# Optimization experiments

Measured on AMD Instinct MI355X. Metric: run time of the kernel, lower is better.

Reference implementation:

```python
import jax, jax.numpy as jnp
import numpy as np
import math

NH, NKV, HD = 8, 1, 128
SOFTCAP = 30.0
ROPE_BASE = 500000.0


def _rope_tables(T, hd, base):
    half = hd // 2
    inv_freq = 1.0 / (base ** (np.arange(half, dtype=np.float32) / half))
    t = np.arange(T, dtype=np.float32)
    ang = np.outer(t, inv_freq)  # [T, half]
    return jnp.asarray(np.cos(ang)), jnp.asarray(np.sin(ang))


def apply_rope(x, cos, sin):
    # x: [B, T, H, hd]; cos/sin: [T, hd//2]
    half = x.shape[-1] // 2
    x1, x2 = x[..., :half], x[..., half:]
    T = x.shape[1]
    c = cos[:T][None, :, None, :]
    s = sin[:T][None, :, None, :]
    return jnp.concatenate([x1 * c - x2 * s, x1 * s + x2 * c], axis=-1)


def setup_inputs() -> dict:
    key = jax.random.key(0)
    ks = jax.random.split(key, 5)
    B, T, D = 4, 2048, 1024
    KD = NKV * HD
    x = jax.random.normal(ks[0], (B, T, D), dtype=jnp.float32)
    Wq = jax.random.normal(ks[1], (D, D), dtype=jnp.float32) * (D ** -0.5)
    Wk = jax.random.normal(ks[2], (KD, D), dtype=jnp.float32) * (D ** -0.5)
    Wv = jax.random.normal(ks[3], (KD, D), dtype=jnp.float32) * (D ** -0.5)
    Wo = jax.random.normal(ks[4], (D, D), dtype=jnp.float32) * (D ** -0.5)
    qk_gain = jnp.full((NH,), 1.5, dtype=jnp.float32)  # qk_gain_init
    cos, sin = _rope_tables(T, HD, ROPE_BASE)
    return {"x": x, "Wq": Wq, "Wk": Wk, "Wv": Wv, "Wo": Wo,
            "qk_gain": qk_gain, "cos": cos, "sin": sin}


def reference(x, Wq, Wk, Wv, Wo, qk_gain, cos, sin):
    B, T, D = x.shape
    # projections (QuantLinear with qat disabled == plain linear, no bias)
    q = (x @ Wq.T).reshape(B, T, NH, HD)
    k = (x @ Wk.T).reshape(B, T, NKV, HD)
    v = (x @ Wv.T).reshape(B, T, NKV, HD)
    q = apply_rope(q, cos, sin)
    k = apply_rope(k, cos, sin)
    # learned per-head QK gain applied to queries
    q = q * qk_gain[None, None, :, 1 - 1][..., None] if False else q * qk_gain[None, None, :, None]
    # GQA: broadcast the single kv head across NH query heads
    scale = 1.0 / math.sqrt(HD)
    scores = jnp.einsum('bqhd,bkgd->bhqk', q, k) * scale  # g==NKV==1 broadcast
    # logit softcap before masking/softmax
    scores = SOFTCAP * jnp.tanh(scores / SOFTCAP)
    causal = jnp.tril(jnp.ones((T, T), dtype=bool))
    scores = jnp.where(causal[None, None], scores, -jnp.inf)
    attn = jax.nn.softmax(scores, axis=-1)  # [B, NH, T, T]
    out = jnp.einsum('bhqk,bkgd->bqhd', attn, v).reshape(B, T, NH * HD)
    return out @ Wo.T
```

## Files before the change

kernel.cpp:

```cpp
#include <hip/hip_runtime.h>
#include <hip/hip_bf16.h>

#define B_ 4
#define T_ 2048
#define D_ 1024
#define NH_ 8
#define HD_ 128

typedef short short8 __attribute__((ext_vector_type(8)));
typedef float floatx4 __attribute__((ext_vector_type(4)));

#if __has_builtin(__builtin_amdgcn_exp2f)
#define EXP2F __builtin_amdgcn_exp2f
#else
#define EXP2F exp2f
#endif
#if __has_builtin(__builtin_amdgcn_rcpf)
#define RCPF __builtin_amdgcn_rcpf
#else
__device__ __forceinline__ float RCPF(float x) { return 1.f / x; }
#endif

#if __has_builtin(__builtin_amdgcn_global_load_lds)
#define G2L(gp, lp)                                                        \
  __builtin_amdgcn_global_load_lds(                                        \
      (const __attribute__((address_space(1))) unsigned int*)(gp),         \
      (__attribute__((address_space(3))) unsigned int*)(lp), 16, 0, 0)
#else
#define G2L(gp, lp) (*(uint4*)(lp) = *(const uint4*)(gp))
#endif

__device__ __forceinline__ unsigned short f2b(float f) {
  union { float fl; unsigned int i; } v; v.fl = f;
  unsigned int r = v.i + 0x7fffu + ((v.i >> 16) & 1u);
  return (unsigned short)(r >> 16);
}
__device__ __forceinline__ unsigned int pack_bf16(float a, float b) {
  unsigned int ua = __float_as_uint(a) + 0x8000u;
  unsigned int ub = __float_as_uint(b) + 0x8000u;
  return (ua >> 16) | (ub & 0xffff0000u);
}
__device__ __forceinline__ float blo(unsigned int u) { return __uint_as_float(u << 16); }
__device__ __forceinline__ float bhi(unsigned int u) { return __uint_as_float(u & 0xffff0000u); }

__global__ __launch_bounds__(256) void cvt_kernel(
    const float* __restrict__ x,  const float* __restrict__ wq,
    const float* __restrict__ wk, const float* __restrict__ wv,
    const float* __restrict__ wo, unsigned short* __restrict__ dst)
{
  size_t i = ((size_t)blockIdx.x * 256 + threadIdx.x) * 8;
  const float* src; size_t off;
  if      (i <  8388608u) { src = x;  off = i; }
  else if (i <  9437184u) { src = wq; off = i - 8388608u; }
  else if (i <  9568256u) { src = wk; off = i - 9437184u; }
  else if (i <  9699328u) { src = wv; off = i - 9568256u; }
  else                    { src = wo; off = i - 9699328u; }
  float4 a = *(const float4*)(src + off);
  float4 b = *(const float4*)(src + off + 4);
  uint4 o;
  o.x = pack_bf16(a.x, a.y); o.y = pack_bf16(a.z, a.w);
  o.z = pack_bf16(b.x, b.y); o.w = pack_bf16(b.z, b.w);
  *(uint4*)(dst + i) = o;
}

template <bool C_F32>
__device__ __forceinline__ void gemm_body_1024(
    const unsigned short* __restrict__ Arow0,
    const unsigned short* __restrict__ Btile,
    void* __restrict__ Cb, int ldC)
{
  __shared__ unsigned short As[128 * 32];
  __shared__ unsigned short Bs[128 * 32];
  const int tid = threadIdx.x;
  const int lane = tid & 63;
  const int w = tid >> 6;
  const int wr = w >> 1, wc = w & 1;
  const int l15 = lane & 15, quad = lane >> 4;

  const unsigned short* a_src = Arow0 + (size_t)(tid >> 2) * 1024 + (tid & 3) * 8;
  const unsigned short* b_src = Btile + (size_t)(tid >> 2) * 1024 + (tid & 3) * 8;
  unsigned short* a_dst = &As[(tid >> 2) * 32 + (tid & 3) * 8];
  unsigned short* b_dst = &Bs[(tid >> 2) * 32 + (tid & 3) * 8];

  floatx4 zero = {0.f, 0.f, 0.f, 0.f};
  floatx4 acc[4][4];
#pragma unroll
  for (int i = 0; i < 4; i++)
#pragma unroll
    for (int j = 0; j < 4; j++) acc[i][j] = zero;

  for (int k0 = 0; k0 < 1024; k0 += 32) {
    __syncthreads();
    G2L(a_src + k0,         a_dst);
    G2L(a_src + 65536 + k0, a_dst + 2048);
    G2L(b_src + k0,         b_dst);
    G2L(b_src + 65536 + k0, b_dst + 2048);
    __syncthreads();
    short8 af[4], bfr[4];
#pragma unroll
    for (int i = 0; i < 4; i++)
      af[i] = *(const short8*)&As[(wr * 64 + i * 16 + l15) * 32 + quad * 8];
#pragma unroll
    for (int j = 0; j < 4; j++)
      bfr[j] = *(const short8*)&Bs[(wc * 64 + j * 16 + l15) * 32 + quad * 8];
#pragma unroll
    for (int i = 0; i < 4; i++)
#pragma unroll
      for (int j = 0; j < 4; j++)
        acc[i][j] = __builtin_amdgcn_mfma_f32_16x16x32_bf16(af[i], bfr[j], acc[i][j], 0, 0, 0);
  }
#pragma unroll
  for (int i = 0; i < 4; i++)
#pragma unroll
    for (int j = 0; j < 4; j++)
#pragma unroll
      for (int r = 0; r < 4; r++) {
        size_t off = (size_t)(wr * 64 + i * 16 + quad * 4 + r) * ldC + wc * 64 + j * 16 + l15;
        if (C_F32) ((float*)Cb)[off] = acc[i][j][r];
        else ((unsigned short*)Cb)[off] = f2b(acc[i][j][r]);
      }
}

__global__ __launch_bounds__(256) void gemm_qkv_kernel(
    const unsigned short* __restrict__ x,
    const unsigned short* __restrict__ Wq,
    const unsigned short* __restrict__ Wk,
    const unsigned short* __restrict__ Wv,
    unsigned short* __restrict__ q,
    unsigned short* __restrict__ k,
    unsigned short* __restrict__ v)
{
  const int bx = blockIdx.x, by = blockIdx.y;
  const unsigned short* Btile;
  unsigned short* C;
  int ldC, col0;
  if (by < 8) { Btile = Wq + (size_t)by * 128 * 1024; C = q; ldC = 1024; col0 = by * 128; }
  else if (by == 8) { Btile = Wk; C = k; ldC = 128; col0 = 0; }
  else { Btile = Wv; C = v; ldC = 128; col0 = 0; }
  gemm_body_1024<false>(x + (size_t)bx * 128 * 1024, Btile,
                        C + (size_t)bx * 128 * ldC + col0, ldC);
}

__global__ __launch_bounds__(256) void gemm_out_kernel(
    const unsigned short* __restrict__ ao,
    const unsigned short* __restrict__ Wo,
    float* __restrict__ out)
{
  const int bx = blockIdx.x, by = blockIdx.y;
  gemm_body_1024<true>(ao + (size_t)bx * 128 * 1024, Wo + (size_t)by * 128 * 1024,
                       out + (size_t)bx * 128 * 1024 + by * 128, 1024);
}

__global__ __launch_bounds__(256) void prep_kernel(
    unsigned short* __restrict__ q,
    unsigned short* __restrict__ k,
    const unsigned short* __restrict__ v,
    unsigned short* __restrict__ vT,
    const float* __restrict__ cosT,
    const float* __restrict__ sinT,
    const float* __restrict__ gain)
{
  __shared__ unsigned short tile[32 * 136];
  const int tid = threadIdx.x;
  if (blockIdx.x < 256) {
    const int b = blockIdx.x >> 6, t0 = (blockIdx.x & 63) * 32;
    for (int u = tid; u < 512; u += 256) {
      int r = u >> 4, c = u & 15;
      *(uint4*)&tile[r * 136 + c * 8] =
          *(const uint4*)(v + ((size_t)(b * T_ + t0 + r)) * 128 + c * 8);
    }
    __syncthreads();
    for (int u = tid; u < 512; u += 256) {
      int d = u >> 2, c = u & 3;
      short8 val;
#pragma unroll
      for (int j = 0; j < 8; j++) val[j] = (short)tile[(c * 8 + j) * 136 + d];
      *(short8*)(vT + ((size_t)(b * 128 + d)) * T_ + t0 + c * 8) = val;
    }
    return;
  }
  int idx = (blockIdx.x - 256) * 256 + tid;
  unsigned short* ptr;
  size_t base;
  int t, j;
  float g;
  if (idx < 524288) {
    j = idx & 7;
    int h = (idx >> 3) & 7;
    int bt = idx >> 6;
    t = bt & (T_ - 1);
    base = (size_t)bt * 1024 + h * 128 + j * 8;
    ptr = q;
    g = gain[h] * 0.0029462782549439484f;
  } else {
    int id = idx - 524288;
    j = id & 7;
    int bt = id >> 3;
    t = bt & (T_ - 1);
    base = (size_t)bt * 128 + j * 8;
    ptr = k;
    g = 1.f;
  }
  float4 ca = *(const float4*)&cosT[t * 64 + j * 8];
  float4 cb = *(const float4*)&cosT[t * 64 + j * 8 + 4];
  float4 sa = *(const float4*)&sinT[t * 64 + j * 8];
  float4 sb = *(const float4*)&sinT[t * 64 + j * 8 + 4];
  uint4 lo = *(const uint4*)(ptr + base);
  uint4 hi = *(const uint4*)(ptr + base + 64);
  uint4 olo, ohi;
  {
    float a0 = blo(lo.x), a1 = bhi(lo.x), b0 = blo(hi.x), b1 = bhi(hi.x);
    olo.x = pack_bf16((a0 * ca.x - b0 * sa.x) * g, (a1 * ca.y - b1 * sa.y) * g);
    ohi.x = pack_bf16((a0 * sa.x + b0 * ca.x) * g, (a1 * sa.y + b1 * ca.y) * g);
  }
  {
    float a0 = blo(lo.y), a1 = bhi(lo.y), b0 = blo(hi.y), b1 = bhi(hi.y);
    olo.y = pack_bf16((a0 * ca.z - b0 * sa.z) * g, (a1 * ca.w - b1 * sa.w) * g);
    ohi.y = pack_bf16((a0 * sa.z + b0 * ca.z) * g, (a1 * sa.w + b1 * ca.w) * g);
  }
  {
    float a0 = blo(lo.z), a1 = bhi(lo.z), b0 = blo(hi.z), b1 = bhi(hi.z);
    olo.z = pack_bf16((a0 * cb.x - b0 * sb.x) * g, (a1 * cb.y - b1 * sb.y) * g);
    ohi.z = pack_bf16((a0 * sb.x + b0 * cb.x) * g, (a1 * sb.y + b1 * cb.y) * g);
  }
  {
    float a0 = blo(lo.w), a1 = bhi(lo.w), b0 = blo(hi.w), b1 = bhi(hi.w);
    olo.w = pack_bf16((a0 * cb.z - b0 * sb.z) * g, (a1 * cb.w - b1 * sb.w) * g);
    ohi.w = pack_bf16((a0 * sb.z + b0 * cb.z) * g, (a1 * sb.w + b1 * cb.w) * g);
  }
  *(uint4*)(ptr + base) = olo;
  *(uint4*)(ptr + base + 64) = ohi;
}

template <int NSPLIT>
__global__ __launch_bounds__(256) void attn_kernel(
    const unsigned short* __restrict__ q,
    const unsigned short* __restrict__ k,
    const unsigned short* __restrict__ vT,
    unsigned short* __restrict__ ao,
    unsigned short* __restrict__ Opart,
    float* __restrict__ lbuf)
{
  __shared__ unsigned short Ks[2][16 * 264];
  __shared__ unsigned short Vts[2][128 * 40];
  __shared__ unsigned short Pw[4][32 * 40];

  const int h = blockIdx.y, b = blockIdx.z;
  const int pr   = blockIdx.x / NSPLIT;
  const int part = blockIdx.x % NSPLIT;
  const int tid = threadIdx.x, lane = tid & 63, w = tid >> 6;
  const int l15 = lane & 15, quad = lane >> 4;

  const unsigned short* ksrc =
      k + (size_t)b * T_ * 128 + (size_t)(tid >> 4) * 128 + (tid & 15) * 8;
  const int koff0 = (tid & 15) * 264 + (tid >> 4) * 8;
  const int koff1 = koff0 + 16 * 8;
  const unsigned short* vsrc =
      vT + (size_t)b * 128 * T_ + (size_t)(tid >> 2) * T_ + (tid & 3) * 8;
  const int voff0 = (tid >> 2) * 40 + (tid & 3) * 8;
  const int voff1 = voff0 + 64 * 40;

  const floatx4 zero = {0.f, 0.f, 0.f, 0.f};

  for (int pass = 0; pass < 2; pass++) {
    const int qblock = pass ? (15 - pr) : pr;
    const int qbase = qblock * 128;
    const int qw = qbase + w * 32;
    const int seg = (4 * qblock + 4) / NSPLIT;
    const int ktBeg = part * seg, ktEnd = ktBeg + seg;

    short8 qf[2][4];
#pragma unroll
    for (int g = 0; g < 2; g++) {
      const unsigned short* qrow =
          q + ((size_t)(b * T_ + qw + g * 16 + l15) * NH_ + h) * HD_;
#pragma unroll
      for (int c = 0; c < 4; c++) qf[g][c] = *(const short8*)(qrow + c * 32 + quad * 8);
    }

    float l_i[2] = {0.f, 0.f};
    floatx4 acc[8][2];
#pragma unroll
    for (int d = 0; d < 8; d++) { acc[d][0] = zero; acc[d][1] = zero; }

    __syncthreads();
    {
      uint4 kr0 = *(const uint4*)(ksrc + (size_t)ktBeg * 4096);
      uint4 kr1 = *(const uint4*)(ksrc + (size_t)ktBeg * 4096 + 2048);
      uint4 vr0 = *(const uint4*)(vsrc + ktBeg * 32);
      uint4 vr1 = *(const uint4*)(vsrc + (size_t)64 * T_ + ktBeg * 32);
      unsigned short* kb = Ks[ktBeg & 1];
      unsigned short* vb = Vts[ktBeg & 1];
      *(uint4*)(kb + koff0) = kr0; *(uint4*)(kb + koff1) = kr1;
      *(uint4*)(vb + voff0) = vr0; *(uint4*)(vb + voff1) = vr1;
    }

    for (int kt = ktBeg; kt < ktEnd; kt++) {
      __syncthreads();
      uint4 kr0, kr1, vr0, vr1;
      const bool more = (kt + 1 < ktEnd);
      if (more) {
        kr0 = *(const uint4*)(ksrc + (size_t)(kt + 1) * 4096);
        kr1 = *(const uint4*)(ksrc + (size_t)(kt + 1) * 4096 + 2048);
        vr0 = *(const uint4*)(vsrc + (kt + 1) * 32);
        vr1 = *(const uint4*)(vsrc + (size_t)64 * T_ + (kt + 1) * 32);
      }

      if (kt * 32 <= qw + 31) {
        const unsigned short* KsC = Ks[kt & 1];
        const unsigned short* VtC = Vts[kt & 1];
        floatx4 st[2][2] = {{zero, zero}, {zero, zero}};
#pragma unroll
        for (int c = 0; c < 4; c++) {
          const int dg = (c * 4 + quad) * 264;
          short8 kf0 = *(const short8*)&KsC[dg + l15 * 8];
          short8 kf1 = *(const short8*)&KsC[dg + (16 + l15) * 8];
          st[0][0] = __builtin_amdgcn_mfma_f32_16x16x32_bf16(kf0, qf[0][c], st[0][0], 0, 0, 0);
          st[0][1] = __builtin_amdgcn_mfma_f32_16x16x32_bf16(kf0, qf[1][c], st[0][1], 0, 0, 0);
          st[1][0] = __builtin_amdgcn_mfma_f32_16x16x32_bf16(kf1, qf[0][c], st[1][0], 0, 0, 0);
          st[1][1] = __builtin_amdgcn_mfma_f32_16x16x32_bf16(kf1, qf[1][c], st[1][1], 0, 0, 0);
        }
        float rs[2] = {0.f, 0.f};
        if (kt * 32 + 31 <= qw) {
#pragma unroll
          for (int f = 0; f < 2; f++)
#pragma unroll
            for (int g = 0; g < 2; g++) {
              float pv[4];
#pragma unroll
              for (int r = 0; r < 4; r++) {
                float s = st[f][g][r];
                float e = EXP2F(2.8853901f * s);
                float u = RCPF(e + 1.f);
                float p = EXP2F(-86.561707f * u);
                pv[r] = p;
                rs[g] += p;
              }
              uint2 pk;
              pk.x = pack_bf16(pv[0], pv[1]);
              pk.y = pack_bf16(pv[2], pv[3]);
              *(uint2*)&Pw[w][(g * 16 + l15) * 40 + f * 16 + quad * 4] = pk;
            }
        } else {
#pragma unroll
          for (int f = 0; f < 2; f++)
#pragma unroll
            for (int g = 0; g < 2; g++) {
              float pv[4];
              const int qrow = qw + g * 16 + l15;
#pragma unroll
              for (int r = 0; r < 4; r++) {
                float s = st[f][g][r];
                float e = EXP2F(2.8853901f * s);
                float u = RCPF(e + 1.f);
                float p = EXP2F(-86.561707f * u);
                int key = kt * 32 + f * 16 + quad * 4 + r;
                p = (key <= qrow) ? p : 0.f;
                pv[r] = p;
                rs[g] += p;
              }
              uint2 pk;
              pk.x = pack_bf16(pv[0], pv[1]);
              pk.y = pack_bf16(pv[2], pv[3]);
              *(uint2*)&Pw[w][(g * 16 + l15) * 40 + f * 16 + quad * 4] = pk;
            }
        }
#pragma unroll
        for (int g = 0; g < 2; g++) {
          float r2 = rs[g] + __shfl_xor(rs[g], 16);
          l_i[g] += r2 + __shfl_xor(r2, 32);
        }
        asm volatile("s_waitcnt lgkmcnt(0)" ::: "memory");
        short8 pf0 = *(const short8*)&Pw[w][l15 * 40 + quad * 8];
        short8 pf1 = *(const short8*)&Pw[w][(16 + l15) * 40 + quad * 8];
#pragma unroll
        for (int d = 0; d < 8; d++) {
          short8 vf = *(const short8*)&VtC[(d * 16 + l15) * 40 + quad * 8];
          acc[d][0] = __builtin_amdgcn_mfma_f32_16x16x32_bf16(vf, pf0, acc[d][0], 0, 0, 0);
          acc[d][1] = __builtin_amdgcn_mfma_f32_16x16x32_bf16(vf, pf1, acc[d][1], 0, 0, 0);
        }
      }

      if (more) {
        unsigned short* kb = Ks[(kt + 1) & 1];
        unsigned short* vb = Vts[(kt + 1) & 1];
        *(uint4*)(kb + koff0) = kr0; *(uint4*)(kb + koff1) = kr1;
        *(uint4*)(vb + voff0) = vr0; *(uint4*)(vb + voff1) = vr1;
      }
    }

#pragma unroll
    for (int g = 0; g < 2; g++) {
      const size_t rowidx = (size_t)(b * T_ + qw + g * 16 + l15) * NH_ + h;
      if (NSPLIT == 1) {
        float linv = 1.f / l_i[g];
        unsigned short* aop = ao + rowidx * HD_ + quad * 4;
#pragma unroll
        for (int d = 0; d < 8; d++) {
          uint2 o;
          o.x = pack_bf16(acc[d][g][0] * linv, acc[d][g][1] * linv);
          o.y = pack_bf16(acc[d][g][2] * linv, acc[d][g][3] * linv);
          *(uint2*)(aop + d * 16) = o;
        }
      } else {
        unsigned short* dst =
            ((part == NSPLIT - 1) ? ao : Opart + (size_t)part * 8388608u) +
            rowidx * HD_ + quad * 4;
#pragma unroll
        for (int d = 0; d < 8; d++) {
          uint2 o;
          o.x = pack_bf16(acc[d][g][0], acc[d][g][1]);
          o.y = pack_bf16(acc[d][g][2], acc[d][g][3]);
          *(uint2*)(dst + d * 16) = o;
        }
        if (quad == 0) lbuf[(size_t)part * 65536u + rowidx] = l_i[g];
      }
    }
  }
}

template <int NSPLIT>
__global__ __launch_bounds__(256) void combine_kernel(
    const unsigned short* __restrict__ Opart,
    const float* __restrict__ lbuf,
    unsigned short* __restrict__ ao)
{
  size_t i = ((size_t)blockIdx.x * 256 + threadIdx.x) * 8;
  size_t r = i >> 7;
  float ls = 0.f;
#pragma unroll
  for (int p = 0; p < NSPLIT; p++) ls += lbuf[(size_t)p * 65536u + r];
  float linv = RCPF(ls);
  uint4 c = *(const uint4*)(ao + i);
  float v0 = blo(c.x), v1 = bhi(c.x), v2 = blo(c.y), v3 = bhi(c.y);
  float v4 = blo(c.z), v5 = bhi(c.z), v6 = blo(c.w), v7 = bhi(c.w);
#pragma unroll
  for (int p = 0; p < NSPLIT - 1; p++) {
    uint4 a = *(const uint4*)(Opart + (size_t)p * 8388608u + i);
    v0 += blo(a.x); v1 += bhi(a.x); v2 += blo(a.y); v3 += bhi(a.y);
    v4 += blo(a.z); v5 += bhi(a.z); v6 += blo(a.w); v7 += bhi(a.w);
  }
  uint4 o;
  o.x = pack_bf16(v0 * linv, v1 * linv);
  o.y = pack_bf16(v2 * linv, v3 * linv);
  o.z = pack_bf16(v4 * linv, v5 * linv);
  o.w = pack_bf16(v6 * linv, v7 * linv);
  *(uint4*)(ao + i) = o;
}

extern "C" void kernel_launch(void* const* d_in, const int* in_sizes, int n_in,
                              void* d_out, int out_size, void* d_ws, size_t ws_size,
                              hipStream_t stream) {
  const float* x    = (const float*)d_in[0];
  const float* Wq   = (const float*)d_in[1];
  const float* Wk   = (const float*)d_in[2];
  const float* Wv   = (const float*)d_in[3];
  const float* Wo   = (const float*)d_in[4];
  const float* gain = (const float*)d_in[5];
  const float* cosT = (const float*)d_in[6];
  const float* sinT = (const float*)d_in[7];
  float* out = (float*)d_out;

  unsigned short* ws = (unsigned short*)d_ws;
  unsigned short* blob = ws;
  unsigned short* xb  = blob;
  unsigned short* Wqb = blob + 8388608u;
  unsigned short* Wkb = blob + 9437184u;
  unsigned short* Wvb = blob + 9568256u;
  unsigned short* Wob = blob + 9699328u;
  unsigned short* q   = ws + 10747904u;
  unsigned short* kk  = ws + 19136512u;
  unsigned short* v   = ws + 20185088u;
  unsigned short* vT  = ws + 21233664u;
  unsigned short* ao  = xb;
  unsigned short* Opart = ws + 22282240u;
  float* l2 = (float*)((char*)d_ws + 61341696u);
  const size_t need2 = 61865984ull;

  cvt_kernel<<<5248, 256, 0, stream>>>(x, Wq, Wk, Wv, Wo, blob);
  gemm_qkv_kernel<<<dim3(64, 10), 256, 0, stream>>>(xb, Wqb, Wkb, Wvb, q, kk, v);
  prep_kernel<<<2560, 256, 0, stream>>>(q, kk, v, vT, cosT, sinT, gain);
  if (ws_size >= need2) {
    attn_kernel<2><<<dim3(16, 8, 4), 256, 0, stream>>>(q, kk, vT, ao, Opart, l2);
    combine_kernel<2><<<4096, 256, 0, stream>>>(Opart, l2, ao);
  } else {
    attn_kernel<1><<<dim3(8, 8, 4), 256, 0, stream>>>(q, kk, vT, ao, Opart, l2);
  }
  gemm_out_kernel<<<dim3(64, 8), 256, 0, stream>>>(ao, Wob, out);
}
```

Measured before the change: 234.2 us.

## Transpose P in registers via permlane swaps and add 4-way KV split

Replaces the LDS round trip used to transpose the probability tile into the PV MFMA operand layout with v_permlane32_swap/v_permlane16_swap register shuffles. This removes the per-wave Pw shared buffer, its writes, the lgkmcnt wait and the reads on every key tile. It also adds an NSPLIT=4 attention path with a combine pass, used when the workspace is large enough, to put more blocks in flight. The extra split costs more partial-output traffic and a heavier combine, and the permlane sequence has to reproduce the old LDS layout exactly to stay correct.

```diff
diff --git a/kernel.cpp b/kernel.cpp
--- a/kernel.cpp
+++ b/kernel.cpp
@@ -243,7 +243,6 @@
 {
   __shared__ unsigned short Ks[2][16 * 264];
   __shared__ unsigned short Vts[2][128 * 40];
-  __shared__ unsigned short Pw[4][32 * 40];
 
   const int h = blockIdx.y, b = blockIdx.z;
   const int pr   = blockIdx.x / NSPLIT;
@@ -321,33 +320,40 @@
           st[1][1] = __builtin_amdgcn_mfma_f32_16x16x32_bf16(kf1, qf[1][c], st[1][1], 0, 0, 0);
         }
         float rs[2] = {0.f, 0.f};
+        short8 pf0, pf1;
         if (kt * 32 + 31 <= qw) {
 #pragma unroll
-          for (int f = 0; f < 2; f++)
-#pragma unroll
-            for (int g = 0; g < 2; g++) {
-              float pv[4];
+          for (int g = 0; g < 2; g++) {
+            float pv[2][4];
+#pragma unroll
+            for (int f = 0; f < 2; f++)
 #pragma unroll
               for (int r = 0; r < 4; r++) {
                 float s = st[f][g][r];
                 float e = EXP2F(2.8853901f * s);
                 float u = RCPF(e + 1.f);
                 float p = EXP2F(-86.561707f * u);
-                pv[r] = p;
+                pv[f][r] = p;
                 rs[g] += p;
               }
-              uint2 pk;
-              pk.x = pack_bf16(pv[0], pv[1]);
-              pk.y = pack_bf16(pv[2], pv[3]);
-              *(uint2*)&Pw[w][(g * 16 + l15) * 40 + f * 16 + quad * 4] = pk;
-            }
+            unsigned int pa = pack_bf16(pv[0][0], pv[0][1]);
+            unsigned int pb = pack_bf16(pv[0][2], pv[0][3]);
+            unsigned int pc = pack_bf16(pv[1][0], pv[1][1]);
+            unsigned int pd = pack_bf16(pv[1][2], pv[1][3]);
+            asm("v_permlane32_swap_b32 %0, %1" : "+v"(pa), "+v"(pc));
+            asm("v_permlane32_swap_b32 %0, %1" : "+v"(pb), "+v"(pd));
+            asm("v_permlane16_swap_b32 %0, %1" : "+v"(pa), "+v"(pc));
+            asm("v_permlane16_swap_b32 %0, %1" : "+v"(pb), "+v"(pd));
+            uint4 u; u.x = pa; u.y = pb; u.z = pc; u.w = pd;
+            (g ? pf1 : pf0) = *(short8*)&u;
+          }
         } else {
 #pragma unroll
-          for (int f = 0; f < 2; f++)
-#pragma unroll
-            for (int g = 0; g < 2; g++) {
-              float pv[4];
-              const int qrow = qw + g * 16 + l15;
+          for (int g = 0; g < 2; g++) {
+            float pv[2][4];
+            const int qrow = qw + g * 16 + l15;
+#pragma unroll
+            for (int f = 0; f < 2; f++)
 #pragma unroll
               for (int r = 0; r < 4; r++) {
                 float s = st[f][g][r];
@@ -356,23 +362,26 @@
                 float p = EXP2F(-86.561707f * u);
                 int key = kt * 32 + f * 16 + quad * 4 + r;
                 p = (key <= qrow) ? p : 0.f;
-                pv[r] = p;
+                pv[f][r] = p;
                 rs[g] += p;
               }
-              uint2 pk;
-              pk.x = pack_bf16(pv[0], pv[1]);
-              pk.y = pack_bf16(pv[2], pv[3]);
-              *(uint2*)&Pw[w][(g * 16 + l15) * 40 + f * 16 + quad * 4] = pk;
-            }
+            unsigned int pa = pack_bf16(pv[0][0], pv[0][1]);
+            unsigned int pb = pack_bf16(pv[0][2], pv[0][3]);
+            unsigned int pc = pack_bf16(pv[1][0], pv[1][1]);
+            unsigned int pd = pack_bf16(pv[1][2], pv[1][3]);
+            asm("v_permlane32_swap_b32 %0, %1" : "+v"(pa), "+v"(pc));
+            asm("v_permlane32_swap_b32 %0, %1" : "+v"(pb), "+v"(pd));
+            asm("v_permlane16_swap_b32 %0, %1" : "+v"(pa), "+v"(pc));
+            asm("v_permlane16_swap_b32 %0, %1" : "+v"(pb), "+v"(pd));
+            uint4 u; u.x = pa; u.y = pb; u.z = pc; u.w = pd;
+            (g ? pf1 : pf0) = *(short8*)&u;
+          }
         }
 #pragma unroll
         for (int g = 0; g < 2; g++) {
           float r2 = rs[g] + __shfl_xor(rs[g], 16);
           l_i[g] += r2 + __shfl_xor(r2, 32);
         }
-        asm volatile("s_waitcnt lgkmcnt(0)" ::: "memory");
-        short8 pf0 = *(const short8*)&Pw[w][l15 * 40 + quad * 8];
-        short8 pf1 = *(const short8*)&Pw[w][(16 + l15) * 40 + quad * 8];
 #pragma unroll
         for (int d = 0; d < 8; d++) {
           short8 vf = *(const short8*)&VtC[(d * 16 + l15) * 40 + quad * 8];
@@ -476,11 +485,16 @@
   unsigned short* Opart = ws + 22282240u;
   float* l2 = (float*)((char*)d_ws + 61341696u);
   const size_t need2 = 61865984ull;
+  float* l4 = (float*)((char*)d_ws + 94896128u);
+  const size_t need4 = 95944704ull;
 
   cvt_kernel<<<5248, 256, 0, stream>>>(x, Wq, Wk, Wv, Wo, blob);
   gemm_qkv_kernel<<<dim3(64, 10), 256, 0, stream>>>(xb, Wqb, Wkb, Wvb, q, kk, v);
   prep_kernel<<<2560, 256, 0, stream>>>(q, kk, v, vT, cosT, sinT, gain);
-  if (ws_size >= need2) {
+  if (ws_size >= need4) {
+    attn_kernel<4><<<dim3(32, 8, 4), 256, 0, stream>>>(q, kk, vT, ao, Opart, l4);
+    combine_kernel<4><<<4096, 256, 0, stream>>>(Opart, l4, ao);
+  } else if (ws_size >= need2) {
     attn_kernel<2><<<dim3(16, 8, 4), 256, 0, stream>>>(q, kk, vT, ao, Opart, l2);
     combine_kernel<2><<<4096, 256, 0, stream>>>(Opart, l2, ao);
   } else {
```

After: 247.4 us. +5.7%, slower.
